# Kernel optimization log

Measured on AMD Instinct MI355X. Metric: run time of the kernel, lower is better.

The kernel has to match this reference:

```python
import jax, jax.numpy as jnp
import numpy as np

# __init__ kwargs
RESCALE_TRANS = 1.0
RESCALE_ROT = 1.0
WEIGHT_PC = 0.5  # weight_point_cloud


def quat2mat(q):
    """Quaternion [w,x,y,z] -> 4x4 homogeneous rotation matrix (LCCNet quat2mat)."""
    q = q / jnp.linalg.norm(q)
    w, x, y, z = q[0], q[1], q[2], q[3]
    return jnp.array([
        [1 - 2*y*y - 2*z*z, 2*x*y - 2*z*w,     2*x*z + 2*y*w,     0.0],
        [2*x*y + 2*z*w,     1 - 2*x*x - 2*z*z, 2*y*z - 2*x*w,     0.0],
        [2*x*z - 2*y*w,     2*y*z + 2*x*w,     1 - 2*x*x - 2*y*y, 0.0],
        [0.0,               0.0,               0.0,               1.0],
    ], dtype=q.dtype)


def tvector2mat(t):
    """Translation vector [3] -> 4x4 homogeneous translation matrix."""
    return jnp.eye(4, dtype=t.dtype).at[:3, 3].set(t)


def quaternion_distance(q, r):
    """Batched angular distance (degrees) between quaternions q,r: [N,4] -> [N]."""
    rinv = r * jnp.array([1.0, -1.0, -1.0, -1.0], dtype=r.dtype)  # conjugate
    # Hamilton product t = q * conj(r)
    w = q[:, 0]*rinv[:, 0] - q[:, 1]*rinv[:, 1] - q[:, 2]*rinv[:, 2] - q[:, 3]*rinv[:, 3]
    x = q[:, 0]*rinv[:, 1] + q[:, 1]*rinv[:, 0] + q[:, 2]*rinv[:, 3] - q[:, 3]*rinv[:, 2]
    y = q[:, 0]*rinv[:, 2] - q[:, 1]*rinv[:, 3] + q[:, 2]*rinv[:, 0] + q[:, 3]*rinv[:, 1]
    z = q[:, 0]*rinv[:, 3] + q[:, 1]*rinv[:, 2] - q[:, 2]*rinv[:, 1] + q[:, 3]*rinv[:, 0]
    angle = 2.0 * jnp.arctan2(jnp.sqrt(x*x + y*y + z*z), jnp.abs(w))
    return 180.0 * angle / jnp.pi


def smooth_l1(pred, tgt):
    """nn.SmoothL1Loss(reduction='none'), beta=1."""
    d = jnp.abs(pred - tgt)
    return jnp.where(d < 1.0, 0.5 * d * d, d - 0.5)


def setup_inputs() -> dict:
    key = jax.random.key(0)
    ks = jax.random.split(key, 5)
    B, N = 32, 200000
    xyz = jax.random.normal(ks[0], (B, 3, N), jnp.float32) * 10.0
    # homogeneous row of ones (points are 4xN homogeneous coords)
    point_clouds = jnp.concatenate([xyz, jnp.ones((B, 1, N), jnp.float32)], axis=1)
    target_transl = jax.random.normal(ks[1], (B, 3), jnp.float32)
    target_rot = jax.random.normal(ks[2], (B, 4), jnp.float32)
    transl_err = jax.random.normal(ks[3], (B, 3), jnp.float32)
    rot_err = jax.random.normal(ks[4], (B, 4), jnp.float32)
    return {
        "point_clouds": point_clouds,
        "target_transl": target_transl,
        "target_rot": target_rot,
        "transl_err": transl_err,
        "rot_err": rot_err,
    }


def reference(point_clouds, target_transl, target_rot, transl_err, rot_err):
    B = target_transl.shape[0]
    # pose loss
    loss_transl = smooth_l1(transl_err, target_transl).sum(axis=1).mean()
    loss_rot = quaternion_distance(rot_err, target_rot).mean()
    pose_loss = RESCALE_TRANS * loss_transl + RESCALE_ROT * loss_rot

    # batched rigid transforms (replaces the per-sample Python loop)
    R_t = jax.vmap(quat2mat)(target_rot)            # [B,4,4]
    T_t = jax.vmap(tvector2mat)(target_transl)      # [B,4,4]
    RT_target = jnp.einsum('bij,bjk->bik', T_t, R_t)
    R_p = jax.vmap(quat2mat)(rot_err)
    T_p = jax.vmap(tvector2mat)(transl_err)
    RT_pred = jnp.einsum('bij,bjk->bik', T_p, R_p)
    RT_total = jnp.einsum('bij,bjk->bik', jnp.linalg.inv(RT_target), RT_pred)
    # rotate_forward applies the INVERSE transform to the 4xN homogeneous points
    RT_inv = jnp.linalg.inv(RT_total)               # [B,4,4]
    pc_out = jnp.einsum('bij,bjn->bin', RT_inv, point_clouds)  # [B,4,N]
    # error.norm(dim=0) over the 4 rows; homogeneous row difference is 0
    err = jnp.linalg.norm(pc_out - point_clouds, axis=1)       # [B,N]
    # (error.clamp(100.0) in the original is not assigned -> no-op)
    point_clouds_loss = err.mean(axis=1).sum()

    total_loss = (1.0 - WEIGHT_PC) * pose_loss + WEIGHT_PC * (point_clouds_loss / B)
    return total_loss, loss_transl, loss_rot, point_clouds_loss / B
```

## Files before the change

### kernel.cpp

```cpp
#include <hip/hip_runtime.h>
#include <math.h>


__device__ inline void quat_to_rot(float q0, float q1, float q2, float q3,
                                   float R[3][3]) {
    float inv_n = rsqrtf(q0 * q0 + q1 * q1 + q2 * q2 + q3 * q3);
    float w = q0 * inv_n, x = q1 * inv_n, y = q2 * inv_n, z = q3 * inv_n;
    R[0][0] = 1.f - 2.f * y * y - 2.f * z * z;
    R[0][1] = 2.f * x * y - 2.f * z * w;
    R[0][2] = 2.f * x * z + 2.f * y * w;
    R[1][0] = 2.f * x * y + 2.f * z * w;
    R[1][1] = 1.f - 2.f * x * x - 2.f * z * z;
    R[1][2] = 2.f * y * z - 2.f * x * w;
    R[2][0] = 2.f * x * z - 2.f * y * w;
    R[2][1] = 2.f * y * z + 2.f * x * w;
    R[2][2] = 1.f - 2.f * x * x - 2.f * y * y;
}

__global__ __launch_bounds__(64) void pose_kernel(
    const float* __restrict__ target_transl, const float* __restrict__ target_rot,
    const float* __restrict__ transl_err, const float* __restrict__ rot_err,
    float* __restrict__ ws, int B) {
    int b = threadIdx.x;
    float s = 0.f, dang = 0.f;
    if (b < B) {
        for (int i = 0; i < 3; i++) {
            float d = fabsf(transl_err[b * 3 + i] - target_transl[b * 3 + i]);
            s += (d < 1.f) ? 0.5f * d * d : d - 0.5f;
        }
        float q0 = rot_err[b * 4 + 0], q1 = rot_err[b * 4 + 1];
        float q2 = rot_err[b * 4 + 2], q3 = rot_err[b * 4 + 3];
        float r0 = target_rot[b * 4 + 0], r1 = -target_rot[b * 4 + 1];
        float r2 = -target_rot[b * 4 + 2], r3 = -target_rot[b * 4 + 3];
        float w = q0 * r0 - q1 * r1 - q2 * r2 - q3 * r3;
        float x = q0 * r1 + q1 * r0 + q2 * r3 - q3 * r2;
        float y = q0 * r2 - q1 * r3 + q2 * r0 + q3 * r1;
        float z = q0 * r3 + q1 * r2 - q2 * r1 + q3 * r0;
        dang = 2.0f * atan2f(sqrtf(x * x + y * y + z * z), fabsf(w)) *
               (180.0f / 3.14159265358979323846f);

        float Rt[3][3], Rp[3][3];
        quat_to_rot(target_rot[b * 4 + 0], target_rot[b * 4 + 1],
                    target_rot[b * 4 + 2], target_rot[b * 4 + 3], Rt);
        quat_to_rot(rot_err[b * 4 + 0], rot_err[b * 4 + 1],
                    rot_err[b * 4 + 2], rot_err[b * 4 + 3], Rp);
        float dt[3];
        for (int k = 0; k < 3; k++)
            dt[k] = target_transl[b * 3 + k] - transl_err[b * 3 + k];
        float* mp = ws + b * 12;
        for (int i = 0; i < 3; i++) {
            for (int j = 0; j < 3; j++) {
                float v = Rp[0][i] * Rt[0][j] + Rp[1][i] * Rt[1][j] +
                          Rp[2][i] * Rt[2][j];
                mp[3 * i + j] = v - (i == j ? 1.f : 0.f);
            }
            mp[9 + i] = Rp[0][i] * dt[0] + Rp[1][i] * dt[1] + Rp[2][i] * dt[2];
        }
    }
    for (int off = 32; off > 0; off >>= 1) {
        s += __shfl_down(s, off);
        dang += __shfl_down(dang, off);
    }
    if (threadIdx.x == 0) {
        ws[12 * B + 0] = s / (float)B;
        ws[12 * B + 1] = dang / (float)B;
        ws[12 * B + 2] = 0.f;
    }
}

__device__ inline float err_pt(float x, float y, float z, float m00, float m01,
                               float m02, float m10, float m11, float m12,
                               float m20, float m21, float m22, float t0,
                               float t1, float t2) {
    float dx = m00 * x + m01 * y + m02 * z + t0;
    float dy = m10 * x + m11 * y + m12 * z + t1;
    float dz = m20 * x + m21 * y + m22 * z + t2;
    return sqrtf(dx * dx + dy * dy + dz * dz);
}

__global__ __launch_bounds__(256) void pc_kernel(const float* __restrict__ pc,
                                                 const float* __restrict__ ws,
                                                 float* __restrict__ acc,
                                                 int N, int B) {
    int b = blockIdx.y;
    const float* mp = ws + b * 12;
    float m00 = mp[0], m01 = mp[1], m02 = mp[2];
    float m10 = mp[3], m11 = mp[4], m12 = mp[5];
    float m20 = mp[6], m21 = mp[7], m22 = mp[8];
    float t0 = mp[9], t1 = mp[10], t2 = mp[11];

    const float* xrow = pc + (size_t)b * 4 * N;
    const float* yrow = xrow + N;
    const float* zrow = yrow + N;

    float local = 0.f;
    if ((N & 3) == 0) {
        int nG = N >> 2;
        const float4* x4p = (const float4*)xrow;
        const float4* y4p = (const float4*)yrow;
        const float4* z4p = (const float4*)zrow;
        for (int g = blockIdx.x * blockDim.x + threadIdx.x; g < nG;
             g += gridDim.x * blockDim.x) {
            float4 x4 = x4p[g], y4 = y4p[g], z4 = z4p[g];
            local += err_pt(x4.x, y4.x, z4.x, m00, m01, m02, m10, m11, m12,
                            m20, m21, m22, t0, t1, t2);
            local += err_pt(x4.y, y4.y, z4.y, m00, m01, m02, m10, m11, m12,
                            m20, m21, m22, t0, t1, t2);
            local += err_pt(x4.z, y4.z, z4.z, m00, m01, m02, m10, m11, m12,
                            m20, m21, m22, t0, t1, t2);
            local += err_pt(x4.w, y4.w, z4.w, m00, m01, m02, m10, m11, m12,
                            m20, m21, m22, t0, t1, t2);
        }
    } else {
        for (int n = blockIdx.x * blockDim.x + threadIdx.x; n < N;
             n += gridDim.x * blockDim.x) {
            local += err_pt(xrow[n], yrow[n], zrow[n], m00, m01, m02, m10, m11,
                            m12, m20, m21, m22, t0, t1, t2);
        }
    }

    __shared__ float smem[4];
    for (int off = 32; off > 0; off >>= 1) local += __shfl_down(local, off);
    int lane = threadIdx.x & 63, wid = threadIdx.x >> 6;
    if (lane == 0) smem[wid] = local;
    __syncthreads();
    if (threadIdx.x == 0) {
        float v = smem[0] + smem[1] + smem[2] + smem[3];
        atomicAdd(acc, v);
    }
}

__global__ __launch_bounds__(64) void final_kernel(const float* __restrict__ ws,
                                                   float* __restrict__ out,
                                                   int B, int N) {
    if (threadIdx.x == 0) {
        float lt = ws[12 * B + 0];
        float lr = ws[12 * B + 1];
        float sum_err = ws[12 * B + 2];
        float pcl = sum_err / (float)N;
        float pclB = pcl / (float)B;
        float pose = lt + lr;
        float total = 0.5f * pose + 0.5f * pclB;
        out[0] = total;
        out[1] = lt;
        out[2] = lr;
        out[3] = pclB;
    }
}

extern "C" void kernel_launch(void* const* d_in, const int* in_sizes, int n_in,
                              void* d_out, int out_size, void* d_ws,
                              size_t ws_size, hipStream_t stream) {
    const float* pc = (const float*)d_in[0];
    const float* target_transl = (const float*)d_in[1];
    const float* target_rot = (const float*)d_in[2];
    const float* transl_err = (const float*)d_in[3];
    const float* rot_err = (const float*)d_in[4];
    float* out = (float*)d_out;
    float* ws = (float*)d_ws;

    int B = in_sizes[1] / 3;
    int N = in_sizes[0] / (4 * B);

    pose_kernel<<<1, 64, 0, stream>>>(target_transl, target_rot, transl_err,
                                      rot_err, ws, B);

    float* acc = ws + 12 * B + 2;
    dim3 grid2(64, B);
    pc_kernel<<<grid2, 256, 0, stream>>>(pc, ws, acc, N, B);

    final_kernel<<<1, 64, 0, stream>>>(ws, out, B, N);
}
```

Measured before the change: 164.3 us.

## Fuse pose setup into point-cloud kernel and replace atomics with partials

Removes the separate pose kernel: each point-cloud block recomputes its batch's 3x4 transform from the quaternions and translations, and the pose losses move into the final reduction kernel. The single global atomicAdd accumulator is replaced by per-block partial sums that the finalize kernel reduces, which also gives a deterministic summation order. This drops one kernel launch and the dependency between launches, at the cost of redundant per-block matrix setup. The main kernel still streams about 77 MB of point data, so its memory-bound cost is unchanged.

```diff
diff --git a/kernel.cpp b/kernel.cpp
--- a/kernel.cpp
+++ b/kernel.cpp
@@ -1,6 +1,8 @@
 #include <hip/hip_runtime.h>
 #include <math.h>
 
+
+#define GX 64
 
 __device__ inline void quat_to_rot(float q0, float q1, float q2, float q3,
                                    float R[3][3]) {
@@ -17,57 +19,6 @@
     R[2][2] = 1.f - 2.f * x * x - 2.f * y * y;
 }
 
-__global__ __launch_bounds__(64) void pose_kernel(
-    const float* __restrict__ target_transl, const float* __restrict__ target_rot,
-    const float* __restrict__ transl_err, const float* __restrict__ rot_err,
-    float* __restrict__ ws, int B) {
-    int b = threadIdx.x;
-    float s = 0.f, dang = 0.f;
-    if (b < B) {
-        for (int i = 0; i < 3; i++) {
-            float d = fabsf(transl_err[b * 3 + i] - target_transl[b * 3 + i]);
-            s += (d < 1.f) ? 0.5f * d * d : d - 0.5f;
-        }
-        float q0 = rot_err[b * 4 + 0], q1 = rot_err[b * 4 + 1];
-        float q2 = rot_err[b * 4 + 2], q3 = rot_err[b * 4 + 3];
-        float r0 = target_rot[b * 4 + 0], r1 = -target_rot[b * 4 + 1];
-        float r2 = -target_rot[b * 4 + 2], r3 = -target_rot[b * 4 + 3];
-        float w = q0 * r0 - q1 * r1 - q2 * r2 - q3 * r3;
-        float x = q0 * r1 + q1 * r0 + q2 * r3 - q3 * r2;
-        float y = q0 * r2 - q1 * r3 + q2 * r0 + q3 * r1;
-        float z = q0 * r3 + q1 * r2 - q2 * r1 + q3 * r0;
-        dang = 2.0f * atan2f(sqrtf(x * x + y * y + z * z), fabsf(w)) *
-               (180.0f / 3.14159265358979323846f);
-
-        float Rt[3][3], Rp[3][3];
-        quat_to_rot(target_rot[b * 4 + 0], target_rot[b * 4 + 1],
-                    target_rot[b * 4 + 2], target_rot[b * 4 + 3], Rt);
-        quat_to_rot(rot_err[b * 4 + 0], rot_err[b * 4 + 1],
-                    rot_err[b * 4 + 2], rot_err[b * 4 + 3], Rp);
-        float dt[3];
-        for (int k = 0; k < 3; k++)
-            dt[k] = target_transl[b * 3 + k] - transl_err[b * 3 + k];
-        float* mp = ws + b * 12;
-        for (int i = 0; i < 3; i++) {
-            for (int j = 0; j < 3; j++) {
-                float v = Rp[0][i] * Rt[0][j] + Rp[1][i] * Rt[1][j] +
-                          Rp[2][i] * Rt[2][j];
-                mp[3 * i + j] = v - (i == j ? 1.f : 0.f);
-            }
-            mp[9 + i] = Rp[0][i] * dt[0] + Rp[1][i] * dt[1] + Rp[2][i] * dt[2];
-        }
-    }
-    for (int off = 32; off > 0; off >>= 1) {
-        s += __shfl_down(s, off);
-        dang += __shfl_down(dang, off);
-    }
-    if (threadIdx.x == 0) {
-        ws[12 * B + 0] = s / (float)B;
-        ws[12 * B + 1] = dang / (float)B;
-        ws[12 * B + 2] = 0.f;
-    }
-}
-
 __device__ inline float err_pt(float x, float y, float z, float m00, float m01,
                                float m02, float m10, float m11, float m12,
                                float m20, float m21, float m22, float t0,
@@ -78,16 +29,32 @@
     return sqrtf(dx * dx + dy * dy + dz * dz);
 }
 
-__global__ __launch_bounds__(256) void pc_kernel(const float* __restrict__ pc,
-                                                 const float* __restrict__ ws,
-                                                 float* __restrict__ acc,
-                                                 int N, int B) {
+__global__ __launch_bounds__(256) void pc_kernel(
+    const float* __restrict__ pc, const float* __restrict__ target_transl,
+    const float* __restrict__ target_rot, const float* __restrict__ transl_err,
+    const float* __restrict__ rot_err, float* __restrict__ partials, int N) {
     int b = blockIdx.y;
-    const float* mp = ws + b * 12;
-    float m00 = mp[0], m01 = mp[1], m02 = mp[2];
-    float m10 = mp[3], m11 = mp[4], m12 = mp[5];
-    float m20 = mp[6], m21 = mp[7], m22 = mp[8];
-    float t0 = mp[9], t1 = mp[10], t2 = mp[11];
+
+    float Rt[3][3], Rp[3][3];
+    quat_to_rot(target_rot[b * 4 + 0], target_rot[b * 4 + 1],
+                target_rot[b * 4 + 2], target_rot[b * 4 + 3], Rt);
+    quat_to_rot(rot_err[b * 4 + 0], rot_err[b * 4 + 1], rot_err[b * 4 + 2],
+                rot_err[b * 4 + 3], Rp);
+    float dt0 = target_transl[b * 3 + 0] - transl_err[b * 3 + 0];
+    float dt1 = target_transl[b * 3 + 1] - transl_err[b * 3 + 1];
+    float dt2 = target_transl[b * 3 + 2] - transl_err[b * 3 + 2];
+    float m00 = Rp[0][0] * Rt[0][0] + Rp[1][0] * Rt[1][0] + Rp[2][0] * Rt[2][0] - 1.f;
+    float m01 = Rp[0][0] * Rt[0][1] + Rp[1][0] * Rt[1][1] + Rp[2][0] * Rt[2][1];
+    float m02 = Rp[0][0] * Rt[0][2] + Rp[1][0] * Rt[1][2] + Rp[2][0] * Rt[2][2];
+    float m10 = Rp[0][1] * Rt[0][0] + Rp[1][1] * Rt[1][0] + Rp[2][1] * Rt[2][0];
+    float m11 = Rp[0][1] * Rt[0][1] + Rp[1][1] * Rt[1][1] + Rp[2][1] * Rt[2][1] - 1.f;
+    float m12 = Rp[0][1] * Rt[0][2] + Rp[1][1] * Rt[1][2] + Rp[2][1] * Rt[2][2];
+    float m20 = Rp[0][2] * Rt[0][0] + Rp[1][2] * Rt[1][0] + Rp[2][2] * Rt[2][0];
+    float m21 = Rp[0][2] * Rt[0][1] + Rp[1][2] * Rt[1][1] + Rp[2][2] * Rt[2][1];
+    float m22 = Rp[0][2] * Rt[0][2] + Rp[1][2] * Rt[1][2] + Rp[2][2] * Rt[2][2] - 1.f;
+    float t0 = Rp[0][0] * dt0 + Rp[1][0] * dt1 + Rp[2][0] * dt2;
+    float t1 = Rp[0][1] * dt0 + Rp[1][1] * dt1 + Rp[2][1] * dt2;
+    float t2 = Rp[0][2] * dt0 + Rp[1][2] * dt1 + Rp[2][2] * dt2;
 
     const float* xrow = pc + (size_t)b * 4 * N;
     const float* yrow = xrow + N;
@@ -100,7 +67,7 @@
         const float4* y4p = (const float4*)yrow;
         const float4* z4p = (const float4*)zrow;
         for (int g = blockIdx.x * blockDim.x + threadIdx.x; g < nG;
-             g += gridDim.x * blockDim.x) {
+             g += GX * blockDim.x) {
             float4 x4 = x4p[g], y4 = y4p[g], z4 = z4p[g];
             local += err_pt(x4.x, y4.x, z4.x, m00, m01, m02, m10, m11, m12,
                             m20, m21, m22, t0, t1, t2);
@@ -113,7 +80,7 @@
         }
     } else {
         for (int n = blockIdx.x * blockDim.x + threadIdx.x; n < N;
-             n += gridDim.x * blockDim.x) {
+             n += GX * blockDim.x) {
             local += err_pt(xrow[n], yrow[n], zrow[n], m00, m01, m02, m10, m11,
                             m12, m20, m21, m22, t0, t1, t2);
         }
@@ -124,24 +91,56 @@
     int lane = threadIdx.x & 63, wid = threadIdx.x >> 6;
     if (lane == 0) smem[wid] = local;
     __syncthreads();
-    if (threadIdx.x == 0) {
-        float v = smem[0] + smem[1] + smem[2] + smem[3];
-        atomicAdd(acc, v);
-    }
+    if (threadIdx.x == 0)
+        partials[blockIdx.y * GX + blockIdx.x] =
+            smem[0] + smem[1] + smem[2] + smem[3];
 }
 
-__global__ __launch_bounds__(64) void final_kernel(const float* __restrict__ ws,
-                                                   float* __restrict__ out,
-                                                   int B, int N) {
+__global__ __launch_bounds__(256) void finalize_kernel(
+    const float* __restrict__ partials, int nPart,
+    const float* __restrict__ target_transl,
+    const float* __restrict__ target_rot,
+    const float* __restrict__ transl_err, const float* __restrict__ rot_err,
+    float* __restrict__ out, int B, int N) {
+    float s = 0.f;
+    for (int i = threadIdx.x; i < nPart; i += 256) s += partials[i];
+    for (int off = 32; off > 0; off >>= 1) s += __shfl_down(s, off);
+    __shared__ float smem[4];
+    int lane = threadIdx.x & 63, wid = threadIdx.x >> 6;
+    if (lane == 0) smem[wid] = s;
+    __syncthreads();
+
+    float st = 0.f, dang = 0.f;
+    int b = threadIdx.x;
+    if (b < B) {
+        for (int i = 0; i < 3; i++) {
+            float d = fabsf(transl_err[b * 3 + i] - target_transl[b * 3 + i]);
+            st += (d < 1.f) ? 0.5f * d * d : d - 0.5f;
+        }
+        float q0 = rot_err[b * 4 + 0], q1 = rot_err[b * 4 + 1];
+        float q2 = rot_err[b * 4 + 2], q3 = rot_err[b * 4 + 3];
+        float r0 = target_rot[b * 4 + 0], r1 = -target_rot[b * 4 + 1];
+        float r2 = -target_rot[b * 4 + 2], r3 = -target_rot[b * 4 + 3];
+        float w = q0 * r0 - q1 * r1 - q2 * r2 - q3 * r3;
+        float x = q0 * r1 + q1 * r0 + q2 * r3 - q3 * r2;
+        float y = q0 * r2 - q1 * r3 + q2 * r0 + q3 * r1;
+        float z = q0 * r3 + q1 * r2 - q2 * r1 + q3 * r0;
+        dang = 2.0f * atan2f(sqrtf(x * x + y * y + z * z), fabsf(w)) *
+               (180.0f / 3.14159265358979323846f);
+    }
+    if (threadIdx.x < 64) {
+        for (int off = 32; off > 0; off >>= 1) {
+            st += __shfl_down(st, off);
+            dang += __shfl_down(dang, off);
+        }
+    }
+
     if (threadIdx.x == 0) {
-        float lt = ws[12 * B + 0];
-        float lr = ws[12 * B + 1];
-        float sum_err = ws[12 * B + 2];
-        float pcl = sum_err / (float)N;
-        float pclB = pcl / (float)B;
-        float pose = lt + lr;
-        float total = 0.5f * pose + 0.5f * pclB;
-        out[0] = total;
+        float sum_err = smem[0] + smem[1] + smem[2] + smem[3];
+        float lt = st / (float)B;
+        float lr = dang / (float)B;
+        float pclB = sum_err / (float)N / (float)B;
+        out[0] = 0.5f * (lt + lr) + 0.5f * pclB;
         out[1] = lt;
         out[2] = lr;
         out[3] = pclB;
@@ -157,17 +156,15 @@
     const float* transl_err = (const float*)d_in[3];
     const float* rot_err = (const float*)d_in[4];
     float* out = (float*)d_out;
-    float* ws = (float*)d_ws;
+    float* partials = (float*)d_ws;
 
     int B = in_sizes[1] / 3;
     int N = in_sizes[0] / (4 * B);
 
-    pose_kernel<<<1, 64, 0, stream>>>(target_transl, target_rot, transl_err,
-                                      rot_err, ws, B);
-
-    float* acc = ws + 12 * B + 2;
-    dim3 grid2(64, B);
-    pc_kernel<<<grid2, 256, 0, stream>>>(pc, ws, acc, N, B);
-
-    final_kernel<<<1, 64, 0, stream>>>(ws, out, B, N);
+    dim3 grid(GX, B);
+    pc_kernel<<<grid, 256, 0, stream>>>(pc, target_transl, target_rot,
+                                        transl_err, rot_err, partials, N);
+    finalize_kernel<<<1, 256, 0, stream>>>(partials, GX * B, target_transl,
+                                           target_rot, transl_err, rot_err,
+                                           out, B, N);
 }
```

Result: faster. 152.1 us (-7.4%).
